# Performance work log

Hardware: AMD Instinct MI355X
Metric: run time of the kernel (lower is better)

## Reference

```python
import jax, jax.numpy as jnp
import numpy as np

N = 2048      # nodes
E = 65536     # edges (avg degree 32)
NV = 6        # n_views (edge_attr dim)
C1, C2, C3 = 32, 32, 32


def _nnconv(x, edge_index, edge_attr, W, b, root, bias, in_c, out_c):
    # Edge MLP: Linear(n_views, in*out) + ReLU -> per-edge weight matrix [E, in, out]
    w = jax.nn.relu(edge_attr @ W + b).reshape(-1, in_c, out_c)
    src, dst = edge_index[0], edge_index[1]  # source_to_target flow
    msg = jnp.einsum('ei,eio->eo', x[src], w)          # gather + edge-specific matmul
    summed = jax.ops.segment_sum(msg, dst, num_segments=N)
    cnt = jax.ops.segment_sum(jnp.ones((msg.shape[0],), x.dtype), dst, num_segments=N)
    agg = summed / jnp.maximum(cnt, 1.0)[:, None]       # scatter-mean (0 for isolated nodes)
    return agg + x @ root + bias                        # root weight + bias (PyG NNConv defaults)


def setup_inputs() -> dict:
    key = jax.random.key(0)
    ks = jax.random.split(key, 12)
    s = 0.1
    return {
        'x': jax.random.normal(ks[0], (N, 1), jnp.float32),
        'edge_attr': jax.random.uniform(ks[1], (E, NV), jnp.float32),
        'edge_index': jax.random.randint(ks[2], (2, E), 0, N, jnp.int64),
        'W1': jax.random.normal(ks[3], (NV, 1 * C1), jnp.float32) * s,
        'b1': jnp.zeros((1 * C1,), jnp.float32),
        'root1': jax.random.normal(ks[4], (1, C1), jnp.float32) * s,
        'bias1': jnp.zeros((C1,), jnp.float32),
        'W2': jax.random.normal(ks[5], (NV, C1 * C2), jnp.float32) * s,
        'b2': jnp.zeros((C1 * C2,), jnp.float32),
        'root2': jax.random.normal(ks[6], (C1, C2), jnp.float32) * s,
        'bias2': jnp.zeros((C2,), jnp.float32),
        'W3': jax.random.normal(ks[7], (NV, C2 * C3), jnp.float32) * s,
        'b3': jnp.zeros((C2 * C3,), jnp.float32),
        'root3': jax.random.normal(ks[8], (C2, C3), jnp.float32) * s,
        'bias3': jnp.zeros((C3,), jnp.float32),
    }


def reference(x, edge_attr, edge_index, W1, b1, root1, bias1, W2, b2, root2, bias2, W3, b3, root3, bias3):
    h = jax.nn.relu(_nnconv(x, edge_index, edge_attr, W1, b1, root1, bias1, 1, C1))
    h = jax.nn.relu(_nnconv(h, edge_index, edge_attr, W2, b2, root2, bias2, C1, C2))
    h = jax.nn.relu(_nnconv(h, edge_index, edge_attr, W3, b3, root3, bias3, C2, C3))
    # CBT: cbt[i, j] = sum_k |h[j, k] - h[i, k]|  (all-pairs L1 distance, [N, N])
    cbt = jnp.sum(jnp.abs(h[None, :, :] - h[:, None, :]), axis=2)
    return cbt
```

## Files before the change

kernel.cpp:

```cpp
#include <hip/hip_runtime.h>

#define N_NODES 2048
#define N_EDGES 65536
#define NV 6
#define C 32
#define BLK 256


__global__ void edge1_kernel(const float* __restrict__ x,
                             const float* __restrict__ ea,
                             const int* __restrict__ src,
                             const int* __restrict__ dst,
                             const float* __restrict__ W1,
                             const float* __restrict__ b1,
                             float* __restrict__ sum1,
                             float* __restrict__ sum23,
                             float* __restrict__ cnt) {
    int t = blockIdx.x * blockDim.x + threadIdx.x;
    if (t < 2 * N_NODES * C) sum23[t] = 0.0f;
    int e = t >> 5, o = t & 31;
    if (e >= N_EDGES) return;
    const float* eap = ea + e * NV;
    float w = b1[o];
#pragma unroll
    for (int v = 0; v < NV; v++) w = fmaf(eap[v], W1[v * C + o], w);
    w = fmaxf(w, 0.0f);
    int d = dst[e];
    atomicAdd(&sum1[d * C + o], x[src[e]] * w);
    if (o == 0) atomicAdd(&cnt[d], 1.0f);
}

template <int IN_C>
__global__ void node_kernel(const float* __restrict__ sum,
                            const float* __restrict__ cnt,
                            const float* __restrict__ hprev,
                            const float* __restrict__ root,
                            const float* __restrict__ bias,
                            float* __restrict__ hout) {
    int t = blockIdx.x * blockDim.x + threadIdx.x;
    int n = t >> 5, o = t & 31;
    float inv = 1.0f / fmaxf(cnt[n], 1.0f);
    float acc = sum[t] * inv + bias[o];
#pragma unroll
    for (int i = 0; i < IN_C; i++) acc = fmaf(hprev[n * IN_C + i], root[i * C + o], acc);
    hout[t] = fmaxf(acc, 0.0f);
}

__global__ __launch_bounds__(BLK, 2) void edge23_kernel(
    const float* __restrict__ hprev,
    const float* __restrict__ ea,
    const int* __restrict__ src,
    const int* __restrict__ dst,
    const float* __restrict__ W,
    const float* __restrict__ b,
    float* __restrict__ sumout)
{
    __shared__ float hb[4][4][256];
    const int lane = threadIdx.x & 63;
    const int o = lane & 31;
    const int half = lane >> 5;
    const int i0 = half * 16;
    const int w = threadIdx.x >> 6;

    float wreg[16][6], breg[16];
#pragma unroll
    for (int j = 0; j < 16; j++) {
#pragma unroll
        for (int v = 0; v < 6; v++) wreg[j][v] = W[v * 1024 + (i0 + j) * C + o];
        breg[j] = b[(i0 + j) * C + o];
    }

    const int wid = (blockIdx.x * BLK + threadIdx.x) >> 6;

    int4 sqs[4];
#pragma unroll
    for (int i = 0; i < 4; i++)
        sqs[i] = *(const int4*)&src[(wid + i * 2048) * 8 + half * 4];
#pragma unroll
    for (int i = 0; i < 4; i++) {
        float4 hq;
        hq.x = hprev[sqs[i].x * C + o];
        hq.y = hprev[sqs[i].y * C + o];
        hq.z = hprev[sqs[i].z * C + o];
        hq.w = hprev[sqs[i].w * C + o];
        *(float4*)&hb[w][i][half * 128 + o * 4] = hq;
    }

#pragma unroll 2
    for (int i = 0; i < 4; i++) {
        const int e0 = (wid + i * 2048) * 8;
        const float* hbw = &hb[w][i][0];
        const float4* eap4 = (const float4*)(ea + (size_t)e0 * NV);
        float accs[8];
#pragma unroll
        for (int sub = 0; sub < 2; sub++) {
            float eaf[24];
#pragma unroll
            for (int t = 0; t < 6; t++) *(float4*)&eaf[t * 4] = eap4[sub * 6 + t];
            float a0 = 0.0f, a1 = 0.0f, a2 = 0.0f, a3 = 0.0f;
#pragma unroll
            for (int j = 0; j < 16; j++) {
                const float4 hA = *(const float4*)&hbw[sub * 128 + (i0 + j) * 4];
                const float bb = breg[j];
                const float w0 = wreg[j][0], w1 = wreg[j][1], w2 = wreg[j][2];
                const float w3 = wreg[j][3], w4 = wreg[j][4], w5 = wreg[j][5];
                float t0 = bb, t1 = bb, t2 = bb, t3 = bb;
                t0 = fmaf(eaf[0],  w0, t0); t1 = fmaf(eaf[6],  w0, t1);
                t2 = fmaf(eaf[12], w0, t2); t3 = fmaf(eaf[18], w0, t3);
                t0 = fmaf(eaf[1],  w1, t0); t1 = fmaf(eaf[7],  w1, t1);
                t2 = fmaf(eaf[13], w1, t2); t3 = fmaf(eaf[19], w1, t3);
                t0 = fmaf(eaf[2],  w2, t0); t1 = fmaf(eaf[8],  w2, t1);
                t2 = fmaf(eaf[14], w2, t2); t3 = fmaf(eaf[20], w2, t3);
                t0 = fmaf(eaf[3],  w3, t0); t1 = fmaf(eaf[9],  w3, t1);
                t2 = fmaf(eaf[15], w3, t2); t3 = fmaf(eaf[21], w3, t3);
                t0 = fmaf(eaf[4],  w4, t0); t1 = fmaf(eaf[10], w4, t1);
                t2 = fmaf(eaf[16], w4, t2); t3 = fmaf(eaf[22], w4, t3);
                t0 = fmaf(eaf[5],  w5, t0); t1 = fmaf(eaf[11], w5, t1);
                t2 = fmaf(eaf[17], w5, t2); t3 = fmaf(eaf[23], w5, t3);
                a0 = fmaf(hA.x, fmaxf(t0, 0.0f), a0);
                a1 = fmaf(hA.y, fmaxf(t1, 0.0f), a1);
                a2 = fmaf(hA.z, fmaxf(t2, 0.0f), a2);
                a3 = fmaf(hA.w, fmaxf(t3, 0.0f), a3);
            }
            accs[sub * 4 + 0] = a0; accs[sub * 4 + 1] = a1;
            accs[sub * 4 + 2] = a2; accs[sub * 4 + 3] = a3;
        }
#pragma unroll
        for (int k = 0; k < 8; k++) accs[k] += __shfl_down(accs[k], 32);

        const int4 dA = *(const int4*)&dst[e0];
        const int4 dB = *(const int4*)&dst[e0 + 4];
        if (lane < 32) {
            atomicAdd(&sumout[dA.x * C + o], accs[0]);
            atomicAdd(&sumout[dA.y * C + o], accs[1]);
            atomicAdd(&sumout[dA.z * C + o], accs[2]);
            atomicAdd(&sumout[dA.w * C + o], accs[3]);
            atomicAdd(&sumout[dB.x * C + o], accs[4]);
            atomicAdd(&sumout[dB.y * C + o], accs[5]);
            atomicAdd(&sumout[dB.z * C + o], accs[6]);
            atomicAdd(&sumout[dB.w * C + o], accs[7]);
        }
    }
}

__global__ __launch_bounds__(BLK) void cbt_kernel(const float* __restrict__ h,
                                                  float* __restrict__ out) {
    __shared__ float hj_s[64][33];
    __shared__ float hi_s[64 * 32];
    const int lane = threadIdx.x & 63;
    const int w = threadIdx.x >> 6;
    const int j0 = blockIdx.x * 64;
    const int i0 = blockIdx.y * 64;
    for (int t = threadIdx.x; t < 64 * 32; t += BLK) {
        hj_s[t >> 5][t & 31] = h[j0 * 32 + t];
        hi_s[t] = h[i0 * 32 + t];
    }
    __syncthreads();
    float hj[32];
#pragma unroll
    for (int k = 0; k < 32; k++) hj[k] = hj_s[lane][k];
    const int j = j0 + lane;
#pragma unroll 4
    for (int ii = w * 16; ii < w * 16 + 16; ii++) {
        float acc = 0.0f;
#pragma unroll
        for (int k = 0; k < 32; k++) acc += fabsf(hi_s[ii * 32 + k] - hj[k]);
        out[(size_t)(i0 + ii) * N_NODES + j] = acc;
    }
}

extern "C" void kernel_launch(void* const* d_in, const int* in_sizes, int n_in,
                              void* d_out, int out_size, void* d_ws, size_t ws_size,
                              hipStream_t stream) {
    const float* x         = (const float*)d_in[0];
    const float* edge_attr = (const float*)d_in[1];
    const int*   edge_idx  = (const int*)d_in[2];
    const float* W1 = (const float*)d_in[3];
    const float* b1 = (const float*)d_in[4];
    const float* root1 = (const float*)d_in[5];
    const float* bias1 = (const float*)d_in[6];
    const float* W2 = (const float*)d_in[7];
    const float* b2 = (const float*)d_in[8];
    const float* root2 = (const float*)d_in[9];
    const float* bias2 = (const float*)d_in[10];
    const float* W3 = (const float*)d_in[11];
    const float* b3 = (const float*)d_in[12];
    const float* root3 = (const float*)d_in[13];
    const float* bias3 = (const float*)d_in[14];

    const int* src = edge_idx;
    const int* dst = edge_idx + N_EDGES;

    float* ws   = (float*)d_ws;
    float* cnt  = ws;
    float* sum1 = ws + N_NODES;
    float* sum2 = sum1 + N_NODES * C;
    float* sum3 = sum2 + N_NODES * C;
    float* h1   = sum3 + N_NODES * C;
    float* h2   = h1 + N_NODES * C;
    float* h3   = h2 + N_NODES * C;

    hipMemsetAsync(d_ws, 0, (size_t)(N_NODES + N_NODES * C) * sizeof(float), stream);

    edge1_kernel<<<(N_EDGES * C) / BLK, BLK, 0, stream>>>(x, edge_attr, src, dst,
                                                          W1, b1, sum1, sum2, cnt);
    node_kernel<1><<<(N_NODES * C) / BLK, BLK, 0, stream>>>(sum1, cnt, x, root1, bias1, h1);

    edge23_kernel<<<512, BLK, 0, stream>>>(h1, edge_attr, src, dst, W2, b2, sum2);
    node_kernel<C><<<(N_NODES * C) / BLK, BLK, 0, stream>>>(sum2, cnt, h1, root2, bias2, h2);

    edge23_kernel<<<512, BLK, 0, stream>>>(h2, edge_attr, src, dst, W3, b3, sum3);
    node_kernel<C><<<(N_NODES * C) / BLK, BLK, 0, stream>>>(sum3, cnt, h2, root3, bias3, h3);

    cbt_kernel<<<dim3(N_NODES / 64, N_NODES / 64), BLK, 0, stream>>>(h3, (float*)d_out);
}
```

Measured before the change: 168.8 us.

## Exploit CBT symmetry, vectorize root loads, spread edge atomics across all lanes

The all-pairs L1 kernel now computes only upper-triangle tiles and writes each result twice, storing the transposed copy through a padded shared-memory tile. This roughly halves the distance arithmetic and the h loads at the cost of extra shared memory and a second strided write pass. In the edge kernel, both halves of the wavefront now issue atomics (xor shuffle plus a select), and the dst loads are hoisted ahead of the compute. The node kernel reads hprev as float4 vectors.

New measurement: 180.9 us. +7.2%, slower.

```diff
diff --git a/kernel.cpp b/kernel.cpp
--- a/kernel.cpp
+++ b/kernel.cpp
@@ -41,8 +41,19 @@
     int n = t >> 5, o = t & 31;
     float inv = 1.0f / fmaxf(cnt[n], 1.0f);
     float acc = sum[t] * inv + bias[o];
-#pragma unroll
-    for (int i = 0; i < IN_C; i++) acc = fmaf(hprev[n * IN_C + i], root[i * C + o], acc);
+    if constexpr (IN_C == 1) {
+        acc = fmaf(hprev[n], root[o], acc);
+    } else {
+        const float4* hp4 = (const float4*)(hprev + n * IN_C);
+#pragma unroll
+        for (int q = 0; q < IN_C / 4; q++) {
+            float4 hv = hp4[q];
+            acc = fmaf(hv.x, root[(q * 4 + 0) * C + o], acc);
+            acc = fmaf(hv.y, root[(q * 4 + 1) * C + o], acc);
+            acc = fmaf(hv.z, root[(q * 4 + 2) * C + o], acc);
+            acc = fmaf(hv.w, root[(q * 4 + 3) * C + o], acc);
+        }
+    }
     hout[t] = fmaxf(acc, 0.0f);
 }
 
@@ -89,6 +100,8 @@
 #pragma unroll 2
     for (int i = 0; i < 4; i++) {
         const int e0 = (wid + i * 2048) * 8;
+        const int4 dA = *(const int4*)&dst[e0];
+        const int4 dB = *(const int4*)&dst[e0 + 4];
         const float* hbw = &hb[w][i][0];
         const float4* eap4 = (const float4*)(ea + (size_t)e0 * NV);
         float accs[8];
@@ -126,31 +139,31 @@
             accs[sub * 4 + 2] = a2; accs[sub * 4 + 3] = a3;
         }
 #pragma unroll
-        for (int k = 0; k < 8; k++) accs[k] += __shfl_down(accs[k], 32);
-
-        const int4 dA = *(const int4*)&dst[e0];
-        const int4 dB = *(const int4*)&dst[e0 + 4];
-        if (lane < 32) {
-            atomicAdd(&sumout[dA.x * C + o], accs[0]);
-            atomicAdd(&sumout[dA.y * C + o], accs[1]);
-            atomicAdd(&sumout[dA.z * C + o], accs[2]);
-            atomicAdd(&sumout[dA.w * C + o], accs[3]);
-            atomicAdd(&sumout[dB.x * C + o], accs[4]);
-            atomicAdd(&sumout[dB.y * C + o], accs[5]);
-            atomicAdd(&sumout[dB.z * C + o], accs[6]);
-            atomicAdd(&sumout[dB.w * C + o], accs[7]);
-        }
+        for (int k = 0; k < 8; k++) accs[k] += __shfl_xor(accs[k], 32);
+
+        const int4 dsel = (lane < 32) ? dA : dB;
+        const float v0 = (lane < 32) ? accs[0] : accs[4];
+        const float v1 = (lane < 32) ? accs[1] : accs[5];
+        const float v2 = (lane < 32) ? accs[2] : accs[6];
+        const float v3 = (lane < 32) ? accs[3] : accs[7];
+        atomicAdd(&sumout[dsel.x * C + o], v0);
+        atomicAdd(&sumout[dsel.y * C + o], v1);
+        atomicAdd(&sumout[dsel.z * C + o], v2);
+        atomicAdd(&sumout[dsel.w * C + o], v3);
     }
 }
 
 __global__ __launch_bounds__(BLK) void cbt_kernel(const float* __restrict__ h,
                                                   float* __restrict__ out) {
+    const int bx = blockIdx.x, by = blockIdx.y;
+    if (by > bx) return;
     __shared__ float hj_s[64][33];
     __shared__ float hi_s[64 * 32];
+    __shared__ float tile[64][65];
     const int lane = threadIdx.x & 63;
     const int w = threadIdx.x >> 6;
-    const int j0 = blockIdx.x * 64;
-    const int i0 = blockIdx.y * 64;
+    const int j0 = bx * 64;
+    const int i0 = by * 64;
     for (int t = threadIdx.x; t < 64 * 32; t += BLK) {
         hj_s[t >> 5][t & 31] = h[j0 * 32 + t];
         hi_s[t] = h[i0 * 32 + t];
@@ -166,6 +179,14 @@
 #pragma unroll
         for (int k = 0; k < 32; k++) acc += fabsf(hi_s[ii * 32 + k] - hj[k]);
         out[(size_t)(i0 + ii) * N_NODES + j] = acc;
+        tile[ii][lane] = acc;
+    }
+    if (by == bx) return;
+    __syncthreads();
+#pragma unroll 4
+    for (int k = 0; k < 16; k++) {
+        const int jj = w * 16 + k;
+        out[(size_t)(j0 + jj) * N_NODES + i0 + lane] = tile[lane][jj];
     }
 }
 
```
